# Kernel tuning notes

Hardware: AMD Instinct MI355X
Metric: run time of the kernel (lower is better)

Reference implementation:

```python
import jax, jax.numpy as jnp
import numpy as np

N_NODES = 1_000_000
N_EDGES = 10_000_000


def gcn_layer(x, src, dst, W, b, n_nodes):
    # Faithful GCNConv: linear transform, symmetric deg^{-1/2} normalization
    # (with self-loops already included in src/dst), scatter-add aggregation, bias.
    xw = x @ W  # [N, out]
    ones = jnp.ones(src.shape[0], dtype=xw.dtype)
    deg = jax.ops.segment_sum(ones, dst, num_segments=n_nodes)  # in-degree incl. self-loop
    d_inv_sqrt = jnp.where(deg > 0, jax.lax.rsqrt(deg), 0.0)
    norm = d_inv_sqrt[src] * d_inv_sqrt[dst]  # [E_total]
    msg = xw[src] * norm[:, None]  # edge-wise gather + scale, [E_total, out]
    out = jax.ops.segment_sum(msg, dst, num_segments=n_nodes)
    return out + b


def setup_inputs() -> dict:
    key = jax.random.key(0)
    k1, k2, k3, k4 = jax.random.split(key, 4)
    x = jax.random.uniform(k1, (N_NODES, 2), dtype=jnp.float32)  # MinMax-scaled feats
    edge_index = jax.random.randint(k2, (2, N_EDGES), 0, N_NODES, dtype=jnp.int64)
    W1 = jax.random.normal(k3, (2, 8), dtype=jnp.float32) * (1.0 / np.sqrt(2.0))
    b1 = jnp.zeros((8,), dtype=jnp.float32)
    W2 = jax.random.normal(k4, (8, 2), dtype=jnp.float32) * (1.0 / np.sqrt(8.0))
    b2 = jnp.zeros((2,), dtype=jnp.float32)
    return {"x": x, "edge_index": edge_index, "W1": W1, "b1": b1, "W2": W2, "b2": b2}


def reference(x, edge_index, W1, b1, W2, b2):
    n_nodes = x.shape[0]
    # GCNConv default: add self-loops before normalization
    loops = jnp.arange(n_nodes, dtype=edge_index.dtype)
    src = jnp.concatenate([edge_index[0], loops])
    dst = jnp.concatenate([edge_index[1], loops])
    h = gcn_layer(x, src, dst, W1, b1, n_nodes)
    h = jax.nn.relu(h)
    out = gcn_layer(h, src, dst, W2, b2, n_nodes)
    return out
```

## Files before the change

### kernel.cpp

```cpp
#include <hip/hip_runtime.h>
#include <hip/hip_fp16.h>


#define NB    1024
#define SHIFT 10
#define WMASK 1023u
#define IDXMASK 0x1FFFFFu
#define EPW   16384
#define BLK   1024
#define MAXLINES ((EPW + 15 * NB) / 16)

typedef unsigned u32x4 __attribute__((ext_vector_type(4)));


__global__ __launch_bounds__(1024) void h_hist(const int* __restrict__ dst, int ne,
                                               int* __restrict__ ghist) {
    __shared__ int h[NB];
    int c = blockIdx.x;
    int c0 = c * EPW, c1 = min(c0 + EPW, ne);
    for (int b = threadIdx.x; b < NB; b += BLK) h[b] = 0;
    __syncthreads();
    int n4 = (c1 - c0) >> 2;
    const int4* d4 = (const int4*)(dst + c0);
    for (int g = threadIdx.x; g < n4; g += BLK) {
        int4 d = d4[g];
        atomicAdd(&h[d.x >> SHIFT], 1);
        atomicAdd(&h[d.y >> SHIFT], 1);
        atomicAdd(&h[d.z >> SHIFT], 1);
        atomicAdd(&h[d.w >> SHIFT], 1);
    }
    for (int e = c0 + (n4 << 2) + threadIdx.x; e < c1; e += BLK)
        atomicAdd(&h[dst[e] >> SHIFT], 1);
    __syncthreads();
    for (int b = threadIdx.x; b < NB; b += BLK)
        ghist[c * NB + b] = (h[b] + 15) & ~15;
}

__global__ void h_colscan(int* __restrict__ ghist, int* __restrict__ tot, int nc) {
    __shared__ int buf[1024];
    int b = blockIdx.x;
    for (int c = threadIdx.x; c < nc; c += blockDim.x) buf[c] = ghist[c * NB + b];
    __syncthreads();
    if (threadIdx.x == 0) {
        int s = 0;
        for (int c = 0; c < nc; ++c) { int v = buf[c]; buf[c] = s; s += v; }
        tot[b] = s;
    }
    __syncthreads();
    for (int c = threadIdx.x; c < nc; c += blockDim.x) ghist[c * NB + b] = buf[c];
}

__global__ void s_scan(const int* __restrict__ tot, int* __restrict__ start) {
    __shared__ int buf[NB];
    int t = threadIdx.x;
    int own = tot[t];
    buf[t] = own;
    __syncthreads();
    for (int off = 1; off < NB; off <<= 1) {
        int add = (t >= off) ? buf[t - off] : 0;
        __syncthreads();
        buf[t] += add;
        __syncthreads();
    }
    start[t] = buf[t] - own;
    if (t == NB - 1) start[NB] = buf[NB - 1];
}

__global__ __launch_bounds__(1024, 2) void h_scatter(
        const int* __restrict__ src, const int* __restrict__ dst, int ne,
        const int* __restrict__ colx, const int* __restrict__ start,
        unsigned* __restrict__ sorted, unsigned sentbase) {
    __shared__ unsigned reorder[EPW];
    __shared__ unsigned short lbase[NB + 1];
    __shared__ unsigned short cbase[NB + 1];
    __shared__ int hist[NB];
    __shared__ int gbase[NB];
    __shared__ unsigned short line_bucket[MAXLINES];

    int c = blockIdx.x;
    int c0 = c * EPW;
    int cnt_edges = min(EPW, ne - c0);
    int t = threadIdx.x;

    hist[t] = 0;
    gbase[t] = start[t] + colx[c * NB + t];
    __syncthreads();

    int n4 = cnt_edges >> 2;
    const int4* d4 = (const int4*)(dst + c0);
    for (int g = t; g < n4; g += BLK) {
        int4 d = d4[g];
        atomicAdd(&hist[d.x >> SHIFT], 1);
        atomicAdd(&hist[d.y >> SHIFT], 1);
        atomicAdd(&hist[d.z >> SHIFT], 1);
        atomicAdd(&hist[d.w >> SHIFT], 1);
    }
    for (int i = (n4 << 2) + t; i < cnt_edges; i += BLK)
        atomicAdd(&hist[dst[c0 + i] >> SHIFT], 1);
    __syncthreads();

    int2* sb = (int2*)reorder;
    int h = hist[t];
    int cap = (h + 15) & ~15;
    sb[t] = make_int2(h, cap);
    __syncthreads();
    for (int o = 1; o < NB; o <<= 1) {
        int2 a = (t >= o) ? sb[t - o] : make_int2(0, 0);
        __syncthreads();
        sb[t].x += a.x; sb[t].y += a.y;
        __syncthreads();
    }
    int lb = sb[t].x - h;
    int cb = sb[t].y - cap;
    lbase[t] = (unsigned short)lb;
    cbase[t] = (unsigned short)cb;
    if (t == NB - 1) {
        lbase[NB] = (unsigned short)sb[t].x;
        cbase[NB] = (unsigned short)sb[t].y;
    }
    for (int k = 0; k < (cap >> 4); ++k)
        line_bucket[(cb >> 4) + k] = (unsigned short)t;
    __syncthreads();
    hist[t] = 0;
    __syncthreads();

    const int4* s4 = (const int4*)(src + c0);
    for (int g = t; g < n4; g += BLK) {
        int4 s = s4[g];
        int4 d = d4[g];
        {
            int b = d.x >> SHIFT; int r = lbase[b] + atomicAdd(&hist[b], 1);
            reorder[r] = ((unsigned)s.x << SHIFT) | ((unsigned)d.x & WMASK);
        }
        {
            int b = d.y >> SHIFT; int r = lbase[b] + atomicAdd(&hist[b], 1);
            reorder[r] = ((unsigned)s.y << SHIFT) | ((unsigned)d.y & WMASK);
        }
        {
            int b = d.z >> SHIFT; int r = lbase[b] + atomicAdd(&hist[b], 1);
            reorder[r] = ((unsigned)s.z << SHIFT) | ((unsigned)d.z & WMASK);
        }
        {
            int b = d.w >> SHIFT; int r = lbase[b] + atomicAdd(&hist[b], 1);
            reorder[r] = ((unsigned)s.w << SHIFT) | ((unsigned)d.w & WMASK);
        }
    }
    for (int i = (n4 << 2) + t; i < cnt_edges; i += BLK) {
        int dd = dst[c0 + i], ss = src[c0 + i];
        int b = dd >> SHIFT; int r = lbase[b] + atomicAdd(&hist[b], 1);
        reorder[r] = ((unsigned)ss << SHIFT) | ((unsigned)dd & WMASK);
    }
    __syncthreads();

    int ptot = cbase[NB];
    for (int p = t; p < ptot; p += BLK) {
        int b = line_bucket[p >> 4];
        int off = p - cbase[b];
        int cnt = lbase[b + 1] - lbase[b];
        unsigned v = (off < cnt) ? reorder[lbase[b] + off]
                                 : (sentbase | (unsigned)(off & WMASK));
        sorted[gbase[b] + off] = v;
    }
}

__global__ void s_deg(const unsigned* __restrict__ sorted, const int* __restrict__ start,
                      const float2* __restrict__ x, float* __restrict__ dinv,
                      __half2* __restrict__ xs, int nn, unsigned sentpad) {
    __shared__ int cnt[NB];
    int b = blockIdx.x;
    for (int i = threadIdx.x; i < NB; i += blockDim.x) cnt[i] = 0;
    __syncthreads();
    int e0 = start[b], e1 = start[b + 1];
    int n4 = (e1 - e0) >> 2;
    const u32x4* sv = (const u32x4*)(sorted + e0);
    int stride2 = blockDim.x * 2;
    for (int g = threadIdx.x; g < n4; g += stride2) {
        int g2 = g + blockDim.x;
        u32x4 a = __builtin_nontemporal_load(sv + g);
        u32x4 b4 = (g2 < n4) ? __builtin_nontemporal_load(sv + g2) : (u32x4)sentpad;
        if (!(a.x >> 31)) atomicAdd(&cnt[a.x & WMASK], 1);
        if (!(a.y >> 31)) atomicAdd(&cnt[a.y & WMASK], 1);
        if (!(a.z >> 31)) atomicAdd(&cnt[a.z & WMASK], 1);
        if (!(a.w >> 31)) atomicAdd(&cnt[a.w & WMASK], 1);
        if (!(b4.x >> 31)) atomicAdd(&cnt[b4.x & WMASK], 1);
        if (!(b4.y >> 31)) atomicAdd(&cnt[b4.y & WMASK], 1);
        if (!(b4.z >> 31)) atomicAdd(&cnt[b4.z & WMASK], 1);
        if (!(b4.w >> 31)) atomicAdd(&cnt[b4.w & WMASK], 1);
    }
    __syncthreads();
    int base = b << SHIFT;
    for (int j = threadIdx.x; j < NB; j += blockDim.x) {
        int node = base + j;
        if (node < nn) {
            float di = rsqrtf((float)(cnt[j] + 1));
            dinv[node] = di;
            float2 xv = x[node];
            xs[node] = __floats2half2_rn(xv.x * di, xv.y * di);
        }
    }
    if (b == 0 && threadIdx.x == 0) xs[nn] = __floats2half2_rn(0.f, 0.f);
}

template <int LAYER>
__global__ void s_agg(const unsigned* __restrict__ sorted, const int* __restrict__ start,
                      const __half2* __restrict__ feat, const float* __restrict__ dinv,
                      const float* __restrict__ W1, const float* __restrict__ b1,
                      const float* __restrict__ W2, const float* __restrict__ b2,
                      __half2* __restrict__ out_h2, float2* __restrict__ out_f2,
                      int nn, unsigned sentpad) {
    __shared__ float accx[NB];
    __shared__ float accy[NB];
    int b = blockIdx.x;
    for (int i = threadIdx.x; i < NB; i += blockDim.x) { accx[i] = 0.f; accy[i] = 0.f; }
    __syncthreads();
    int e0 = start[b], e1 = start[b + 1];
    int n4 = (e1 - e0) >> 2;
    const u32x4* sv = (const u32x4*)(sorted + e0);
    int stride2 = blockDim.x * 2;
    for (int g = threadIdx.x; g < n4; g += stride2) {
        int g2 = g + blockDim.x;
        u32x4 a = __builtin_nontemporal_load(sv + g);
        u32x4 c = (g2 < n4) ? __builtin_nontemporal_load(sv + g2) : (u32x4)sentpad;
        float2 f0 = __half22float2(feat[(a.x >> SHIFT) & IDXMASK]);
        float2 f1 = __half22float2(feat[(a.y >> SHIFT) & IDXMASK]);
        float2 f2 = __half22float2(feat[(a.z >> SHIFT) & IDXMASK]);
        float2 f3 = __half22float2(feat[(a.w >> SHIFT) & IDXMASK]);
        float2 f4 = __half22float2(feat[(c.x >> SHIFT) & IDXMASK]);
        float2 f5 = __half22float2(feat[(c.y >> SHIFT) & IDXMASK]);
        float2 f6 = __half22float2(feat[(c.z >> SHIFT) & IDXMASK]);
        float2 f7 = __half22float2(feat[(c.w >> SHIFT) & IDXMASK]);
        if (!(a.x >> 31)) { atomicAdd(&accx[a.x & WMASK], f0.x); atomicAdd(&accy[a.x & WMASK], f0.y); }
        if (!(a.y >> 31)) { atomicAdd(&accx[a.y & WMASK], f1.x); atomicAdd(&accy[a.y & WMASK], f1.y); }
        if (!(a.z >> 31)) { atomicAdd(&accx[a.z & WMASK], f2.x); atomicAdd(&accy[a.z & WMASK], f2.y); }
        if (!(a.w >> 31)) { atomicAdd(&accx[a.w & WMASK], f3.x); atomicAdd(&accy[a.w & WMASK], f3.y); }
        if (!(c.x >> 31)) { atomicAdd(&accx[c.x & WMASK], f4.x); atomicAdd(&accy[c.x & WMASK], f4.y); }
        if (!(c.y >> 31)) { atomicAdd(&accx[c.y & WMASK], f5.x); atomicAdd(&accy[c.y & WMASK], f5.y); }
        if (!(c.z >> 31)) { atomicAdd(&accx[c.z & WMASK], f6.x); atomicAdd(&accy[c.z & WMASK], f6.y); }
        if (!(c.w >> 31)) { atomicAdd(&accx[c.w & WMASK], f7.x); atomicAdd(&accy[c.w & WMASK], f7.y); }
    }
    __syncthreads();
    int base = b << SHIFT;
    for (int j = threadIdx.x; j < NB; j += blockDim.x) {
        int node = base + j;
        if (node >= nn) continue;
        float di = dinv[node];
        float2 self = __half22float2(feat[node]);
        float ax = di * (accx[j] + self.x);
        float ay = di * (accy[j] + self.y);
        if (LAYER == 1) {
            float o0 = 0.f, o1 = 0.f;
#pragma unroll
            for (int k = 0; k < 8; ++k) {
                float hk = fmaxf(ax * W1[k] + ay * W1[8 + k] + b1[k], 0.f);
                o0 += hk * W2[2 * k + 0];
                o1 += hk * W2[2 * k + 1];
            }
            out_h2[node] = __floats2half2_rn(o0 * di, o1 * di);
        } else {
            float2 r = make_float2(ax + b2[0], ay + b2[1]);
            __builtin_nontemporal_store(r.x, &out_f2[node].x);
            __builtin_nontemporal_store(r.y, &out_f2[node].y);
        }
    }
    if (LAYER == 1 && b == 0 && threadIdx.x == 0)
        out_h2[nn] = __floats2half2_rn(0.f, 0.f);
}


__global__ void k_deg(const int* __restrict__ dst, int* __restrict__ deg, int ne) {
    int i = blockIdx.x * blockDim.x + threadIdx.x;
    int stride = gridDim.x * blockDim.x;
    for (; i < ne; i += stride) atomicAdd(&deg[dst[i]], 1);
}
__global__ void k_dinv(const int* __restrict__ deg, float* __restrict__ dinv, int nn) {
    int i = blockIdx.x * blockDim.x + threadIdx.x;
    if (i < nn) dinv[i] = rsqrtf((float)(deg[i] + 1));
}
__global__ void k_edge2(const int* __restrict__ src, const int* __restrict__ dst,
                        const float* __restrict__ feat2, const float* __restrict__ dinv,
                        float* __restrict__ agg2, int ne) {
    int i = blockIdx.x * blockDim.x + threadIdx.x;
    int stride = gridDim.x * blockDim.x;
    for (; i < ne; i += stride) {
        int s = src[i], d = dst[i];
        float nrm = dinv[s] * dinv[d];
        float2 f = reinterpret_cast<const float2*>(feat2)[s];
        unsafeAtomicAdd(&agg2[2 * d + 0], nrm * f.x);
        unsafeAtomicAdd(&agg2[2 * d + 1], nrm * f.y);
    }
}
__global__ void k_mid(const float* __restrict__ x, const float* __restrict__ aggx,
                      const float* __restrict__ dinv,
                      const float* __restrict__ W1, const float* __restrict__ b1,
                      const float* __restrict__ W2, float* __restrict__ a2, int nn) {
    int i = blockIdx.x * blockDim.x + threadIdx.x;
    if (i >= nn) return;
    float di = dinv[i], di2 = di * di;
    float2 xsv = reinterpret_cast<const float2*>(x)[i];
    float ax = aggx[2 * i + 0] + di2 * xsv.x;
    float ay = aggx[2 * i + 1] + di2 * xsv.y;
    float o0 = 0.f, o1 = 0.f;
#pragma unroll
    for (int k = 0; k < 8; ++k) {
        float hk = fmaxf(ax * W1[k] + ay * W1[8 + k] + b1[k], 0.f);
        o0 += hk * W2[2 * k + 0];
        o1 += hk * W2[2 * k + 1];
    }
    a2[2 * i + 0] = o0;
    a2[2 * i + 1] = o1;
}
__global__ void k_out(const float* __restrict__ a2, const float* __restrict__ dinv,
                      const float* __restrict__ b2, float* __restrict__ out, int nn) {
    int i = blockIdx.x * blockDim.x + threadIdx.x;
    if (i >= nn) return;
    float di = dinv[i], di2 = di * di;
    out[2 * i + 0] = out[2 * i + 0] + di2 * a2[2 * i + 0] + b2[0];
    out[2 * i + 1] = out[2 * i + 1] + di2 * a2[2 * i + 1] + b2[1];
}

extern "C" void kernel_launch(void* const* d_in, const int* in_sizes, int n_in,
                              void* d_out, int out_size, void* d_ws, size_t ws_size,
                              hipStream_t stream) {
    const float* x  = (const float*)d_in[0];
    const int*   ei = (const int*)d_in[1];
    const float* W1 = (const float*)d_in[2];
    const float* b1 = (const float*)d_in[3];
    const float* W2 = (const float*)d_in[4];
    const float* b2 = (const float*)d_in[5];
    float* out = (float*)d_out;

    const int nn = in_sizes[0] / 2;
    const int ne = in_sizes[1] / 2;
    const int* src = ei;
    const int* dst = ei + ne;

    char* ws = (char*)d_ws;
    size_t off = 0;
    auto alloc = [&](size_t bytes) -> void* {
        void* p = ws + off;
        off += (bytes + 255) & ~size_t(255);
        return p;
    };

    int nc = (ne + EPW - 1) / EPW;
    size_t sorted_elems = (size_t)ne + (size_t)nc * NB * 16;
    size_t need = sorted_elems * 4 + (size_t)nn * 4 + 2 * ((size_t)nn + 1) * 4
                + (size_t)nc * NB * 4 + (2 * NB + 2) * 4 + 16384;

    if (ws_size >= need && nc <= 1024) {
        unsigned* sorted = (unsigned*)alloc(sorted_elems * 4);
        float*    dinv   = (float*)   alloc((size_t)nn * 4);
        __half2*  xs     = (__half2*) alloc(((size_t)nn + 1) * 4);
        __half2*  xs2    = (__half2*) alloc(((size_t)nn + 1) * 4);
        int*      ghist  = (int*)     alloc((size_t)nc * NB * 4);
        int*      tot    = (int*)     alloc(NB * 4);
        int*      start  = (int*)     alloc((NB + 1) * 4);

        unsigned sentbase = 0x80000000u | ((unsigned)nn << SHIFT);

        h_hist   <<<nc, BLK, 0, stream>>>(dst, ne, ghist);
        h_colscan<<<NB, 256, 0, stream>>>(ghist, tot, nc);
        s_scan   <<<1, NB, 0, stream>>>(tot, start);
        h_scatter<<<nc, BLK, 0, stream>>>(src, dst, ne, ghist, start, sorted, sentbase);
        s_deg    <<<NB, 512, 0, stream>>>(sorted, start, (const float2*)x, dinv, xs, nn,
                                          sentbase);
        s_agg<1> <<<NB, 512, 0, stream>>>(sorted, start, xs, dinv, W1, b1, W2, b2,
                                          xs2, nullptr, nn, sentbase);
        s_agg<2> <<<NB, 512, 0, stream>>>(sorted, start, xs2, dinv, W1, b1, W2, b2,
                                          nullptr, (float2*)out, nn, sentbase);
    } else {
        int*   deg  = (int*)  alloc((size_t)nn * 4);
        float* dinv = (float*)alloc((size_t)nn * 4);
        float* aggx = (float*)alloc((size_t)nn * 8);
        float* a2   = (float*)alloc((size_t)nn * 8);
        hipMemsetAsync(deg,  0, (size_t)nn * 4, stream);
        hipMemsetAsync(aggx, 0, (size_t)nn * 8, stream);
        hipMemsetAsync(d_out, 0, (size_t)nn * 8, stream);
        const int TB = 256;
        int egrid = (ne + TB - 1) / TB;
        int ngrid = (nn + TB - 1) / TB;
        k_deg  <<<egrid, TB, 0, stream>>>(dst, deg, ne);
        k_dinv <<<ngrid, TB, 0, stream>>>(deg, dinv, nn);
        k_edge2<<<egrid, TB, 0, stream>>>(src, dst, x, dinv, aggx, ne);
        k_mid  <<<ngrid, TB, 0, stream>>>(x, aggx, dinv, W1, b1, W2, a2, nn);
        k_edge2<<<egrid, TB, 0, stream>>>(src, dst, a2, dinv, out, ne);
        k_out  <<<ngrid, TB, 0, stream>>>(a2, dinv, b2, out, nn);
    }
}
```

Before: 310.4 us.

## Reuse per-chunk histogram in scatter and batch loads in degree/aggregation kernels

h_hist now stores raw per-chunk bucket counts, so h_scatter reads them instead of recomputing the histogram. This removes one full pass over dst and its shared-memory atomics. s_deg and s_agg switch to per-thread contiguous batches of 8 vector loads, issuing all feature gathers before the atomics to raise memory-level parallelism, and gain launch_bounds(512,4). The costs are an extra nc*NB count array, higher register pressure, and a less coalesced per-thread-contiguous access pattern.

```diff
diff --git a/kernel.cpp b/kernel.cpp
--- a/kernel.cpp
+++ b/kernel.cpp
@@ -9,12 +9,14 @@
 #define EPW   16384
 #define BLK   1024
 #define MAXLINES ((EPW + 15 * NB) / 16)
+#define BATCH 8
 
 typedef unsigned u32x4 __attribute__((ext_vector_type(4)));
 
 
 __global__ __launch_bounds__(1024) void h_hist(const int* __restrict__ dst, int ne,
-                                               int* __restrict__ ghist) {
+                                               int* __restrict__ ghist,
+                                               int* __restrict__ cnts) {
     __shared__ int h[NB];
     int c = blockIdx.x;
     int c0 = c * EPW, c1 = min(c0 + EPW, ne);
@@ -32,8 +34,11 @@
     for (int e = c0 + (n4 << 2) + threadIdx.x; e < c1; e += BLK)
         atomicAdd(&h[dst[e] >> SHIFT], 1);
     __syncthreads();
-    for (int b = threadIdx.x; b < NB; b += BLK)
-        ghist[c * NB + b] = (h[b] + 15) & ~15;
+    for (int b = threadIdx.x; b < NB; b += BLK) {
+        int v = h[b];
+        cnts [c * NB + b] = v;
+        ghist[c * NB + b] = (v + 15) & ~15;
+    }
 }
 
 __global__ void h_colscan(int* __restrict__ ghist, int* __restrict__ tot, int nc) {
@@ -66,9 +71,10 @@
     if (t == NB - 1) start[NB] = buf[NB - 1];
 }
 
-__global__ __launch_bounds__(1024, 2) void h_scatter(
+__global__ __launch_bounds__(1024) void h_scatter(
         const int* __restrict__ src, const int* __restrict__ dst, int ne,
-        const int* __restrict__ colx, const int* __restrict__ start,
+        const int* __restrict__ colx, const int* __restrict__ cnts,
+        const int* __restrict__ start,
         unsigned* __restrict__ sorted, unsigned sentbase) {
     __shared__ unsigned reorder[EPW];
     __shared__ unsigned short lbase[NB + 1];
@@ -82,25 +88,12 @@
     int cnt_edges = min(EPW, ne - c0);
     int t = threadIdx.x;
 
-    hist[t] = 0;
+    int h = cnts[c * NB + t];
+    hist[t] = h;
     gbase[t] = start[t] + colx[c * NB + t];
     __syncthreads();
 
-    int n4 = cnt_edges >> 2;
-    const int4* d4 = (const int4*)(dst + c0);
-    for (int g = t; g < n4; g += BLK) {
-        int4 d = d4[g];
-        atomicAdd(&hist[d.x >> SHIFT], 1);
-        atomicAdd(&hist[d.y >> SHIFT], 1);
-        atomicAdd(&hist[d.z >> SHIFT], 1);
-        atomicAdd(&hist[d.w >> SHIFT], 1);
-    }
-    for (int i = (n4 << 2) + t; i < cnt_edges; i += BLK)
-        atomicAdd(&hist[dst[c0 + i] >> SHIFT], 1);
-    __syncthreads();
-
     int2* sb = (int2*)reorder;
-    int h = hist[t];
     int cap = (h + 15) & ~15;
     sb[t] = make_int2(h, cap);
     __syncthreads();
@@ -124,7 +117,9 @@
     hist[t] = 0;
     __syncthreads();
 
+    int n4 = cnt_edges >> 2;
     const int4* s4 = (const int4*)(src + c0);
+    const int4* d4 = (const int4*)(dst + c0);
     for (int g = t; g < n4; g += BLK) {
         int4 s = s4[g];
         int4 d = d4[g];
@@ -163,9 +158,10 @@
     }
 }
 
-__global__ void s_deg(const unsigned* __restrict__ sorted, const int* __restrict__ start,
-                      const float2* __restrict__ x, float* __restrict__ dinv,
-                      __half2* __restrict__ xs, int nn, unsigned sentpad) {
+__global__ __launch_bounds__(512, 4) void s_deg(
+        const unsigned* __restrict__ sorted, const int* __restrict__ start,
+        const float2* __restrict__ x, float* __restrict__ dinv,
+        __half2* __restrict__ xs, int nn, unsigned sentpad) {
     __shared__ int cnt[NB];
     int b = blockIdx.x;
     for (int i = threadIdx.x; i < NB; i += blockDim.x) cnt[i] = 0;
@@ -173,19 +169,21 @@
     int e0 = start[b], e1 = start[b + 1];
     int n4 = (e1 - e0) >> 2;
     const u32x4* sv = (const u32x4*)(sorted + e0);
-    int stride2 = blockDim.x * 2;
-    for (int g = threadIdx.x; g < n4; g += stride2) {
-        int g2 = g + blockDim.x;
-        u32x4 a = __builtin_nontemporal_load(sv + g);
-        u32x4 b4 = (g2 < n4) ? __builtin_nontemporal_load(sv + g2) : (u32x4)sentpad;
-        if (!(a.x >> 31)) atomicAdd(&cnt[a.x & WMASK], 1);
-        if (!(a.y >> 31)) atomicAdd(&cnt[a.y & WMASK], 1);
-        if (!(a.z >> 31)) atomicAdd(&cnt[a.z & WMASK], 1);
-        if (!(a.w >> 31)) atomicAdd(&cnt[a.w & WMASK], 1);
-        if (!(b4.x >> 31)) atomicAdd(&cnt[b4.x & WMASK], 1);
-        if (!(b4.y >> 31)) atomicAdd(&cnt[b4.y & WMASK], 1);
-        if (!(b4.z >> 31)) atomicAdd(&cnt[b4.z & WMASK], 1);
-        if (!(b4.w >> 31)) atomicAdd(&cnt[b4.w & WMASK], 1);
+    for (int qb = 0; qb < n4; qb += 512 * BATCH) {
+        int base_q = qb + threadIdx.x * BATCH;
+        u32x4 q[BATCH];
+#pragma unroll
+        for (int i = 0; i < BATCH; ++i) {
+            int g = base_q + i;
+            q[i] = (g < n4) ? __builtin_nontemporal_load(sv + g) : (u32x4)sentpad;
+        }
+#pragma unroll
+        for (int i = 0; i < BATCH; ++i) {
+            if (!(q[i].x >> 31)) atomicAdd(&cnt[q[i].x & WMASK], 1);
+            if (!(q[i].y >> 31)) atomicAdd(&cnt[q[i].y & WMASK], 1);
+            if (!(q[i].z >> 31)) atomicAdd(&cnt[q[i].z & WMASK], 1);
+            if (!(q[i].w >> 31)) atomicAdd(&cnt[q[i].w & WMASK], 1);
+        }
     }
     __syncthreads();
     int base = b << SHIFT;
@@ -202,12 +200,13 @@
 }
 
 template <int LAYER>
-__global__ void s_agg(const unsigned* __restrict__ sorted, const int* __restrict__ start,
-                      const __half2* __restrict__ feat, const float* __restrict__ dinv,
-                      const float* __restrict__ W1, const float* __restrict__ b1,
-                      const float* __restrict__ W2, const float* __restrict__ b2,
-                      __half2* __restrict__ out_h2, float2* __restrict__ out_f2,
-                      int nn, unsigned sentpad) {
+__global__ __launch_bounds__(512, 4) void s_agg(
+        const unsigned* __restrict__ sorted, const int* __restrict__ start,
+        const __half2* __restrict__ feat, const float* __restrict__ dinv,
+        const float* __restrict__ W1, const float* __restrict__ b1,
+        const float* __restrict__ W2, const float* __restrict__ b2,
+        __half2* __restrict__ out_h2, float2* __restrict__ out_f2,
+        int nn, unsigned sentpad) {
     __shared__ float accx[NB];
     __shared__ float accy[NB];
     int b = blockIdx.x;
@@ -216,27 +215,36 @@
     int e0 = start[b], e1 = start[b + 1];
     int n4 = (e1 - e0) >> 2;
     const u32x4* sv = (const u32x4*)(sorted + e0);
-    int stride2 = blockDim.x * 2;
-    for (int g = threadIdx.x; g < n4; g += stride2) {
-        int g2 = g + blockDim.x;
-        u32x4 a = __builtin_nontemporal_load(sv + g);
-        u32x4 c = (g2 < n4) ? __builtin_nontemporal_load(sv + g2) : (u32x4)sentpad;
-        float2 f0 = __half22float2(feat[(a.x >> SHIFT) & IDXMASK]);
-        float2 f1 = __half22float2(feat[(a.y >> SHIFT) & IDXMASK]);
-        float2 f2 = __half22float2(feat[(a.z >> SHIFT) & IDXMASK]);
-        float2 f3 = __half22float2(feat[(a.w >> SHIFT) & IDXMASK]);
-        float2 f4 = __half22float2(feat[(c.x >> SHIFT) & IDXMASK]);
-        float2 f5 = __half22float2(feat[(c.y >> SHIFT) & IDXMASK]);
-        float2 f6 = __half22float2(feat[(c.z >> SHIFT) & IDXMASK]);
-        float2 f7 = __half22float2(feat[(c.w >> SHIFT) & IDXMASK]);
-        if (!(a.x >> 31)) { atomicAdd(&accx[a.x & WMASK], f0.x); atomicAdd(&accy[a.x & WMASK], f0.y); }
-        if (!(a.y >> 31)) { atomicAdd(&accx[a.y & WMASK], f1.x); atomicAdd(&accy[a.y & WMASK], f1.y); }
-        if (!(a.z >> 31)) { atomicAdd(&accx[a.z & WMASK], f2.x); atomicAdd(&accy[a.z & WMASK], f2.y); }
-        if (!(a.w >> 31)) { atomicAdd(&accx[a.w & WMASK], f3.x); atomicAdd(&accy[a.w & WMASK], f3.y); }
-        if (!(c.x >> 31)) { atomicAdd(&accx[c.x & WMASK], f4.x); atomicAdd(&accy[c.x & WMASK], f4.y); }
-        if (!(c.y >> 31)) { atomicAdd(&accx[c.y & WMASK], f5.x); atomicAdd(&accy[c.y & WMASK], f5.y); }
-        if (!(c.z >> 31)) { atomicAdd(&accx[c.z & WMASK], f6.x); atomicAdd(&accy[c.z & WMASK], f6.y); }
-        if (!(c.w >> 31)) { atomicAdd(&accx[c.w & WMASK], f7.x); atomicAdd(&accy[c.w & WMASK], f7.y); }
+    const unsigned* featu = (const unsigned*)feat;
+    for (int qb = 0; qb < n4; qb += 512 * BATCH) {
+        int base_q = qb + threadIdx.x * BATCH;
+        u32x4 q[BATCH];
+#pragma unroll
+        for (int i = 0; i < BATCH; ++i) {
+            int g = base_q + i;
+            q[i] = (g < n4) ? __builtin_nontemporal_load(sv + g) : (u32x4)sentpad;
+        }
+        unsigned fv[BATCH][4];
+#pragma unroll
+        for (int i = 0; i < BATCH; ++i) {
+            fv[i][0] = featu[(q[i].x >> SHIFT) & IDXMASK];
+            fv[i][1] = featu[(q[i].y >> SHIFT) & IDXMASK];
+            fv[i][2] = featu[(q[i].z >> SHIFT) & IDXMASK];
+            fv[i][3] = featu[(q[i].w >> SHIFT) & IDXMASK];
+        }
+#pragma unroll
+        for (int i = 0; i < BATCH; ++i) {
+            unsigned e[4] = {q[i].x, q[i].y, q[i].z, q[i].w};
+#pragma unroll
+            for (int k = 0; k < 4; ++k) {
+                if (!(e[k] >> 31)) {
+                    float2 f = __half22float2(*(const __half2*)&fv[i][k]);
+                    int j = e[k] & WMASK;
+                    atomicAdd(&accx[j], f.x);
+                    atomicAdd(&accy[j], f.y);
+                }
+            }
+        }
     }
     __syncthreads();
     int base = b << SHIFT;
@@ -345,7 +353,7 @@
     int nc = (ne + EPW - 1) / EPW;
     size_t sorted_elems = (size_t)ne + (size_t)nc * NB * 16;
     size_t need = sorted_elems * 4 + (size_t)nn * 4 + 2 * ((size_t)nn + 1) * 4
-                + (size_t)nc * NB * 4 + (2 * NB + 2) * 4 + 16384;
+                + 2 * (size_t)nc * NB * 4 + (2 * NB + 2) * 4 + 16384;
 
     if (ws_size >= need && nc <= 1024) {
         unsigned* sorted = (unsigned*)alloc(sorted_elems * 4);
@@ -353,15 +361,17 @@
         __half2*  xs     = (__half2*) alloc(((size_t)nn + 1) * 4);
         __half2*  xs2    = (__half2*) alloc(((size_t)nn + 1) * 4);
         int*      ghist  = (int*)     alloc((size_t)nc * NB * 4);
+        int*      cnts   = (int*)     alloc((size_t)nc * NB * 4);
         int*      tot    = (int*)     alloc(NB * 4);
         int*      start  = (int*)     alloc((NB + 1) * 4);
 
         unsigned sentbase = 0x80000000u | ((unsigned)nn << SHIFT);
 
-        h_hist   <<<nc, BLK, 0, stream>>>(dst, ne, ghist);
+        h_hist   <<<nc, BLK, 0, stream>>>(dst, ne, ghist, cnts);
         h_colscan<<<NB, 256, 0, stream>>>(ghist, tot, nc);
         s_scan   <<<1, NB, 0, stream>>>(tot, start);
-        h_scatter<<<nc, BLK, 0, stream>>>(src, dst, ne, ghist, start, sorted, sentbase);
+        h_scatter<<<nc, BLK, 0, stream>>>(src, dst, ne, ghist, cnts, start, sorted,
+                                          sentbase);
         s_deg    <<<NB, 512, 0, stream>>>(sorted, start, (const float2*)x, dinv, xs, nn,
                                           sentbase);
         s_agg<1> <<<NB, 512, 0, stream>>>(sorted, start, xs, dinv, W1, b1, W2, b2,
```

Measured after the change: 378.0 us. +21.8%, slower.

## Reuse per-chunk histogram in scatter and widen bucket kernels to 1024 threads

Applied to the files above, without the earlier changes.

h_hist now writes the raw per-chunk bucket counts to a new cnts buffer, and h_scatter reads those counts instead of recomputing the histogram. This removes a full pass over dst and its shared-memory atomics from h_scatter. The scatter kernel also drops its min-blocks-per-CU launch bound. s_deg and s_agg now launch with 1024 threads per block instead of 512. The cost is an extra nc*NB int array written and read back, and different occupancy and register limits for the larger blocks.

```diff
diff --git a/kernel.cpp b/kernel.cpp
--- a/kernel.cpp
+++ b/kernel.cpp
@@ -14,7 +14,8 @@
 
 
 __global__ __launch_bounds__(1024) void h_hist(const int* __restrict__ dst, int ne,
-                                               int* __restrict__ ghist) {
+                                               int* __restrict__ ghist,
+                                               int* __restrict__ cnts) {
     __shared__ int h[NB];
     int c = blockIdx.x;
     int c0 = c * EPW, c1 = min(c0 + EPW, ne);
@@ -32,8 +33,11 @@
     for (int e = c0 + (n4 << 2) + threadIdx.x; e < c1; e += BLK)
         atomicAdd(&h[dst[e] >> SHIFT], 1);
     __syncthreads();
-    for (int b = threadIdx.x; b < NB; b += BLK)
-        ghist[c * NB + b] = (h[b] + 15) & ~15;
+    for (int b = threadIdx.x; b < NB; b += BLK) {
+        int v = h[b];
+        cnts [c * NB + b] = v;
+        ghist[c * NB + b] = (v + 15) & ~15;
+    }
 }
 
 __global__ void h_colscan(int* __restrict__ ghist, int* __restrict__ tot, int nc) {
@@ -66,9 +70,10 @@
     if (t == NB - 1) start[NB] = buf[NB - 1];
 }
 
-__global__ __launch_bounds__(1024, 2) void h_scatter(
+__global__ __launch_bounds__(1024) void h_scatter(
         const int* __restrict__ src, const int* __restrict__ dst, int ne,
-        const int* __restrict__ colx, const int* __restrict__ start,
+        const int* __restrict__ colx, const int* __restrict__ cnts,
+        const int* __restrict__ start,
         unsigned* __restrict__ sorted, unsigned sentbase) {
     __shared__ unsigned reorder[EPW];
     __shared__ unsigned short lbase[NB + 1];
@@ -82,25 +87,12 @@
     int cnt_edges = min(EPW, ne - c0);
     int t = threadIdx.x;
 
-    hist[t] = 0;
+    int h = cnts[c * NB + t];
+    hist[t] = h;
     gbase[t] = start[t] + colx[c * NB + t];
     __syncthreads();
 
-    int n4 = cnt_edges >> 2;
-    const int4* d4 = (const int4*)(dst + c0);
-    for (int g = t; g < n4; g += BLK) {
-        int4 d = d4[g];
-        atomicAdd(&hist[d.x >> SHIFT], 1);
-        atomicAdd(&hist[d.y >> SHIFT], 1);
-        atomicAdd(&hist[d.z >> SHIFT], 1);
-        atomicAdd(&hist[d.w >> SHIFT], 1);
-    }
-    for (int i = (n4 << 2) + t; i < cnt_edges; i += BLK)
-        atomicAdd(&hist[dst[c0 + i] >> SHIFT], 1);
-    __syncthreads();
-
     int2* sb = (int2*)reorder;
-    int h = hist[t];
     int cap = (h + 15) & ~15;
     sb[t] = make_int2(h, cap);
     __syncthreads();
@@ -124,7 +116,9 @@
     hist[t] = 0;
     __syncthreads();
 
+    int n4 = cnt_edges >> 2;
     const int4* s4 = (const int4*)(src + c0);
+    const int4* d4 = (const int4*)(dst + c0);
     for (int g = t; g < n4; g += BLK) {
         int4 s = s4[g];
         int4 d = d4[g];
@@ -163,9 +157,10 @@
     }
 }
 
-__global__ void s_deg(const unsigned* __restrict__ sorted, const int* __restrict__ start,
-                      const float2* __restrict__ x, float* __restrict__ dinv,
-                      __half2* __restrict__ xs, int nn, unsigned sentpad) {
+__global__ __launch_bounds__(1024) void s_deg(
+        const unsigned* __restrict__ sorted, const int* __restrict__ start,
+        const float2* __restrict__ x, float* __restrict__ dinv,
+        __half2* __restrict__ xs, int nn, unsigned sentpad) {
     __shared__ int cnt[NB];
     int b = blockIdx.x;
     for (int i = threadIdx.x; i < NB; i += blockDim.x) cnt[i] = 0;
@@ -202,12 +197,13 @@
 }
 
 template <int LAYER>
-__global__ void s_agg(const unsigned* __restrict__ sorted, const int* __restrict__ start,
-                      const __half2* __restrict__ feat, const float* __restrict__ dinv,
-                      const float* __restrict__ W1, const float* __restrict__ b1,
-                      const float* __restrict__ W2, const float* __restrict__ b2,
-                      __half2* __restrict__ out_h2, float2* __restrict__ out_f2,
-                      int nn, unsigned sentpad) {
+__global__ __launch_bounds__(1024) void s_agg(
+        const unsigned* __restrict__ sorted, const int* __restrict__ start,
+        const __half2* __restrict__ feat, const float* __restrict__ dinv,
+        const float* __restrict__ W1, const float* __restrict__ b1,
+        const float* __restrict__ W2, const float* __restrict__ b2,
+        __half2* __restrict__ out_h2, float2* __restrict__ out_f2,
+        int nn, unsigned sentpad) {
     __shared__ float accx[NB];
     __shared__ float accy[NB];
     int b = blockIdx.x;
@@ -345,7 +341,7 @@
     int nc = (ne + EPW - 1) / EPW;
     size_t sorted_elems = (size_t)ne + (size_t)nc * NB * 16;
     size_t need = sorted_elems * 4 + (size_t)nn * 4 + 2 * ((size_t)nn + 1) * 4
-                + (size_t)nc * NB * 4 + (2 * NB + 2) * 4 + 16384;
+                + 2 * (size_t)nc * NB * 4 + (2 * NB + 2) * 4 + 16384;
 
     if (ws_size >= need && nc <= 1024) {
         unsigned* sorted = (unsigned*)alloc(sorted_elems * 4);
@@ -353,21 +349,23 @@
         __half2*  xs     = (__half2*) alloc(((size_t)nn + 1) * 4);
         __half2*  xs2    = (__half2*) alloc(((size_t)nn + 1) * 4);
         int*      ghist  = (int*)     alloc((size_t)nc * NB * 4);
+        int*      cnts   = (int*)     alloc((size_t)nc * NB * 4);
         int*      tot    = (int*)     alloc(NB * 4);
         int*      start  = (int*)     alloc((NB + 1) * 4);
 
         unsigned sentbase = 0x80000000u | ((unsigned)nn << SHIFT);
 
-        h_hist   <<<nc, BLK, 0, stream>>>(dst, ne, ghist);
+        h_hist   <<<nc, BLK, 0, stream>>>(dst, ne, ghist, cnts);
         h_colscan<<<NB, 256, 0, stream>>>(ghist, tot, nc);
         s_scan   <<<1, NB, 0, stream>>>(tot, start);
-        h_scatter<<<nc, BLK, 0, stream>>>(src, dst, ne, ghist, start, sorted, sentbase);
-        s_deg    <<<NB, 512, 0, stream>>>(sorted, start, (const float2*)x, dinv, xs, nn,
+        h_scatter<<<nc, BLK, 0, stream>>>(src, dst, ne, ghist, cnts, start, sorted,
                                           sentbase);
-        s_agg<1> <<<NB, 512, 0, stream>>>(sorted, start, xs, dinv, W1, b1, W2, b2,
-                                          xs2, nullptr, nn, sentbase);
-        s_agg<2> <<<NB, 512, 0, stream>>>(sorted, start, xs2, dinv, W1, b1, W2, b2,
-                                          nullptr, (float2*)out, nn, sentbase);
+        s_deg    <<<NB, 1024, 0, stream>>>(sorted, start, (const float2*)x, dinv, xs, nn,
+                                           sentbase);
+        s_agg<1> <<<NB, 1024, 0, stream>>>(sorted, start, xs, dinv, W1, b1, W2, b2,
+                                           xs2, nullptr, nn, sentbase);
+        s_agg<2> <<<NB, 1024, 0, stream>>>(sorted, start, xs2, dinv, W1, b1, W2, b2,
+                                           nullptr, (float2*)out, nn, sentbase);
     } else {
         int*   deg  = (int*)  alloc((size_t)nn * 4);
         float* dinv = (float*)alloc((size_t)nn * 4);
```

New measurement: 308.9 us. No clear change (-0.5%).
